# Optimization experiments

Measured on AMD Instinct MI355X. Metric: run time of the kernel, lower is better.

Reference implementation:

```python
import jax, jax.numpy as jnp
import numpy as np

NUM_HEADS = 16
HIDDEN = 64  # per-head dim


def setup_inputs() -> dict:
    key = jax.random.key(0)
    ks = jax.random.split(key, 7)
    B, Nq, S, D = 2, 2048, 2048, 1024
    return {
        "queries": jax.random.normal(ks[0], (B, Nq, D), jnp.float32),
        "keys": jax.random.normal(ks[1], (B, S, D), jnp.float32),
        "values": jax.random.normal(ks[2], (B, S, D), jnp.float32),
        "Wq": jax.random.normal(ks[3], (D, NUM_HEADS * HIDDEN), jnp.float32) * 0.02,
        "Wk": jax.random.normal(ks[4], (D, NUM_HEADS * HIDDEN), jnp.float32) * 0.02,
        "Wv": jax.random.normal(ks[5], (D, NUM_HEADS * HIDDEN), jnp.float32) * 0.02,
        "Wo": jax.random.normal(ks[6], (NUM_HEADS * HIDDEN, 1024), jnp.float32) * 0.02,
    }


def reference(queries, keys, values, Wq, Wk, Wv, Wo):
    B, Nq, _ = queries.shape
    S = keys.shape[1]
    H, dh = NUM_HEADS, HIDDEN
    # projections, split heads: [B, len, H, dh] -> [B, H, len, dh]
    Q = (queries @ Wq).reshape(B, Nq, H, dh).transpose(0, 2, 1, 3)
    K = (keys @ Wk).reshape(B, S, H, dh).transpose(0, 2, 1, 3)
    V = (values @ Wv).reshape(B, S, H, dh).transpose(0, 2, 1, 3)
    scores = jnp.einsum("bhqd,bhkd->bhqk", Q, K) / jnp.sqrt(jnp.float32(dh))
    # NOTE: faithful to original -- softmax over ALL keys, THEN multiply by
    # strictly-lower-triangular mask (triangular * (1 - diagonal)); no renorm.
    P = jax.nn.softmax(scores, axis=-1)
    mask = jnp.tril(jnp.ones((Nq, S), jnp.float32), -1)  # strict lower triangle
    Sout = jnp.einsum("bhqk,bhkd->bhqd", P * mask, V)
    merged = Sout.transpose(0, 2, 1, 3).reshape(B, Nq, H * dh)
    return merged @ Wo
```

## Files before the change

### kernel.cpp

```cpp
#include <hip/hip_runtime.h>
#include <hip/hip_bf16.h>
#include <stdint.h>


typedef __bf16 bf16x8 __attribute__((ext_vector_type(8)));
typedef float f32x4 __attribute__((ext_vector_type(4)));

typedef const __attribute__((address_space(1))) void* gas_t;
typedef __attribute__((address_space(3))) void* las_t;

__device__ __forceinline__ unsigned short f2bf(float f) {
    unsigned int u = __float_as_uint(f);
    return (unsigned short)((u + 0x7FFFu + ((u >> 16) & 1u)) >> 16);
}

__global__ __launch_bounds__(256) void cast_qkv(
    const float* __restrict__ q, const float* __restrict__ k, const float* __restrict__ v,
    unsigned short* __restrict__ oq, unsigned short* __restrict__ ok, unsigned short* __restrict__ ov)
{
    const float* src = (blockIdx.z == 0) ? q : (blockIdx.z == 1) ? k : v;
    unsigned short* dst = (blockIdx.z == 0) ? oq : (blockIdx.z == 1) ? ok : ov;
    unsigned int i = blockIdx.x * 256u + threadIdx.x;
    float4 f = reinterpret_cast<const float4*>(src)[i];
    ushort4 o;
    o.x = f2bf(f.x); o.y = f2bf(f.y); o.z = f2bf(f.z); o.w = f2bf(f.w);
    reinterpret_cast<ushort4*>(dst)[i] = o;
}

__global__ __launch_bounds__(256) void transpose_w(
    const float* __restrict__ w0, const float* __restrict__ w1,
    const float* __restrict__ w2, const float* __restrict__ w3,
    unsigned short* __restrict__ t0, unsigned short* __restrict__ t1,
    unsigned short* __restrict__ t2, unsigned short* __restrict__ t3)
{
    const float* W = (blockIdx.z == 0) ? w0 : (blockIdx.z == 1) ? w1 : (blockIdx.z == 2) ? w2 : w3;
    unsigned short* T = (blockIdx.z == 0) ? t0 : (blockIdx.z == 1) ? t1 : (blockIdx.z == 2) ? t2 : t3;
    __shared__ float s[32][33];
    const int tx = threadIdx.x, ty = threadIdx.y;
    const int x = blockIdx.x * 32 + tx;
#pragma unroll
    for (int j = 0; j < 4; ++j)
        s[ty + 8 * j][tx] = W[(size_t)(blockIdx.y * 32 + ty + 8 * j) * 1024 + x];
    __syncthreads();
    const int xo = blockIdx.y * 32 + tx;
#pragma unroll
    for (int j = 0; j < 4; ++j)
        T[(size_t)(blockIdx.x * 32 + ty + 8 * j) * 1024 + xo] = f2bf(s[tx][ty + 8 * j]);
}

template <int BM, int BN, int MODE>
__global__ __launch_bounds__(256) void gemm_bt(
    const unsigned short* __restrict__ A0, const unsigned short* __restrict__ A1,
    const unsigned short* __restrict__ A2,
    const unsigned short* __restrict__ B0, const unsigned short* __restrict__ B1,
    const unsigned short* __restrict__ B2,
    unsigned short* __restrict__ C0, unsigned short* __restrict__ C1,
    unsigned short* __restrict__ C2, float* __restrict__ Cf)
{
    constexpr int K = 1024;
    constexpr int WM = BM / 2, WN = BN / 2, MI = WM / 16, NI = WN / 16;
    __shared__ __align__(16) unsigned char lds[(BM + BN) * 64];
    unsigned char* lA = lds;
    unsigned char* lB = lds + BM * 64;

    const int tid = threadIdx.x;
    const int z = blockIdx.z;
    const unsigned short* A  = (MODE == 1 || z == 0) ? A0 : (z == 1) ? A1 : A2;
    const unsigned short* Bt = (MODE == 1 || z == 0) ? B0 : (z == 1) ? B1 : B2;
    const int m0 = blockIdx.y * BM, n0 = blockIdx.x * BN;
    const int w = tid >> 6, lane = tid & 63, g = lane >> 4, l15 = lane & 15;
    const int wr = w >> 1, wc = w & 1;

    f32x4 acc[MI][NI] = {};

    for (int k0 = 0; k0 < K; k0 += 32) {
#pragma unroll
        for (int r = 0; r < (BM * 64) / 4096; ++r) {
            const int o = (r * 256 + tid) * 16;
            const unsigned char* gp = (const unsigned char*)A
                + ((size_t)(m0 + (o >> 6)) * K + k0) * 2 + (o & 63);
            __builtin_amdgcn_global_load_lds((gas_t)gp,
                (las_t)(lA + (r * 256 + (tid & ~63)) * 16), 16, 0, 0);
        }
#pragma unroll
        for (int r = 0; r < (BN * 64) / 4096; ++r) {
            const int o = (r * 256 + tid) * 16;
            const unsigned char* gp = (const unsigned char*)Bt
                + ((size_t)(n0 + (o >> 6)) * K + k0) * 2 + (o & 63);
            __builtin_amdgcn_global_load_lds((gas_t)gp,
                (las_t)(lB + (r * 256 + (tid & ~63)) * 16), 16, 0, 0);
        }
        __syncthreads();

        bf16x8 a[MI], bfr[NI];
#pragma unroll
        for (int mi = 0; mi < MI; ++mi)
            a[mi] = *(const bf16x8*)(lA + (wr * WM + mi * 16 + l15) * 64 + g * 16);
#pragma unroll
        for (int ni = 0; ni < NI; ++ni)
            bfr[ni] = *(const bf16x8*)(lB + (wc * WN + ni * 16 + l15) * 64 + g * 16);
#pragma unroll
        for (int mi = 0; mi < MI; ++mi)
#pragma unroll
            for (int ni = 0; ni < NI; ++ni)
                acc[mi][ni] = __builtin_amdgcn_mfma_f32_16x16x32_bf16(a[mi], bfr[ni], acc[mi][ni], 0, 0, 0);
        __syncthreads();
    }

    if (MODE == 1) {
#pragma unroll
        for (int mi = 0; mi < MI; ++mi)
#pragma unroll
            for (int ni = 0; ni < NI; ++ni)
#pragma unroll
                for (int i = 0; i < 4; ++i) {
                    const int row = m0 + wr * WM + mi * 16 + 4 * g + i;
                    const int col = n0 + wc * WN + ni * 16 + l15;
                    Cf[(size_t)row * 1024 + col] = acc[mi][ni][i];
                }
    } else if (z < 2) {
        unsigned short* C = (z == 0) ? C0 : C1;
#pragma unroll
        for (int mi = 0; mi < MI; ++mi)
#pragma unroll
            for (int ni = 0; ni < NI; ++ni)
#pragma unroll
                for (int i = 0; i < 4; ++i) {
                    const int row = m0 + wr * WM + mi * 16 + 4 * g + i;
                    const int col = n0 + wc * WN + ni * 16 + l15;
                    C[(size_t)row * 1024 + col] = f2bf(acc[mi][ni][i]);
                }
    } else {
#pragma unroll
        for (int mi = 0; mi < MI; ++mi)
#pragma unroll
            for (int ni = 0; ni < NI; ++ni)
#pragma unroll
                for (int i = 0; i < 4; ++i) {
                    const int row = m0 + wr * WM + mi * 16 + 4 * g + i;
                    const int col = n0 + wc * WN + ni * 16 + l15;
                    const int b = row >> 11, s = row & 2047;
                    const int hh = col >> 6, d = col & 63;
                    C2[(((size_t)b * 16 + hh) * 64 + d) * 2048 + s] = f2bf(acc[mi][ni][i]);
                }
    }
}

__global__ __launch_bounds__(256) void attn_kernel(
    const unsigned short* __restrict__ Qp, const unsigned short* __restrict__ Kp,
    const unsigned short* __restrict__ Vt, unsigned short* __restrict__ mrg)
{
    __shared__ __align__(16) unsigned char lds[24576];
    unsigned char* Ks = lds;
    unsigned char* Vs = lds + 8192;
    unsigned char* Ps = lds + 16384;

    const int tid = threadIdx.x;
    const int w = tid >> 6, lane = tid & 63, g = lane >> 4, l15 = lane & 15;
    const int qt = blockIdx.x, h = blockIdx.y, b = blockIdx.z;
    const int q0 = qt * 64;
    const int bh = b * 16 + h;

    bf16x8 aq[2];
    {
        const unsigned short* qp = Qp + ((size_t)(b * 2048 + q0 + 16 * w + l15) * 1024 + h * 64 + g * 8);
        aq[0] = *(const bf16x8*)qp;
        aq[1] = *(const bf16x8*)(qp + 32);
    }

    f32x4 oacc[4] = {};
    float denom[4] = {0.f, 0.f, 0.f, 0.f};

    for (int k0 = 0; k0 < 2048; k0 += 64) {
        const bool do_pv = (k0 < q0 + 64);
#pragma unroll
        for (int r = 0; r < 2; ++r) {
            const int o = (r * 256 + tid) * 16;
            const int row = o >> 7;
            const uint4 vv = *(const uint4*)((const unsigned char*)Kp
                + ((size_t)(b * 2048 + k0 + row) * 1024 + h * 64) * 2 + (o & 127));
            *(uint4*)(Ks + (o ^ ((row & 7) << 4))) = vv;
        }
        if (do_pv) {
#pragma unroll
            for (int r = 0; r < 2; ++r) {
                const int o = (r * 256 + tid) * 16;
                const int row = o >> 7;
                const uint4 vv = *(const uint4*)((const unsigned char*)Vt
                    + (((size_t)bh * 64 + row) * 2048 + k0) * 2 + (o & 127));
                *(uint4*)(Vs + (o ^ ((row & 7) << 4))) = vv;
            }
        }
        __syncthreads();

        f32x4 pe[4];
#pragma unroll
        for (int ni = 0; ni < 4; ++ni) {
            const int row = ni * 16 + l15;
            const int sw = (row & 7) << 4;
            const bf16x8 bk0 = *(const bf16x8*)(Ks + ((row * 128 + g * 16) ^ sw));
            const bf16x8 bk1 = *(const bf16x8*)(Ks + ((row * 128 + 64 + g * 16) ^ sw));
            f32x4 t = {};
            t = __builtin_amdgcn_mfma_f32_16x16x32_bf16(aq[0], bk0, t, 0, 0, 0);
            t = __builtin_amdgcn_mfma_f32_16x16x32_bf16(aq[1], bk1, t, 0, 0, 0);
#pragma unroll
            for (int i = 0; i < 4; ++i)
                pe[ni][i] = __expf(t[i] * 0.125f);
        }
#pragma unroll
        for (int i = 0; i < 4; ++i) {
            float rs = pe[0][i] + pe[1][i] + pe[2][i] + pe[3][i];
            rs += __shfl_xor(rs, 1, 64);
            rs += __shfl_xor(rs, 2, 64);
            rs += __shfl_xor(rs, 4, 64);
            rs += __shfl_xor(rs, 8, 64);
            denom[i] += rs;
        }
        if (do_pv) {
#pragma unroll
            for (int ni = 0; ni < 4; ++ni)
#pragma unroll
                for (int i = 0; i < 4; ++i) {
                    const int row = 16 * w + 4 * g + i;
                    const int colg = k0 + ni * 16 + l15;
                    const unsigned short pv =
                        (colg < q0 + row) ? f2bf(pe[ni][i]) : (unsigned short)0;
                    *(unsigned short*)(Ps + ((row * 128 + (ni * 16 + l15) * 2) ^ ((row & 7) << 4))) = pv;
                }
            __syncthreads();
#pragma unroll
            for (int kk = 0; kk < 2; ++kk) {
                const int rowp = 16 * w + l15;
                const bf16x8 pa = *(const bf16x8*)(Ps + ((rowp * 128 + kk * 64 + g * 16) ^ ((rowp & 7) << 4)));
#pragma unroll
                for (int ni = 0; ni < 4; ++ni) {
                    const int rv = ni * 16 + l15;
                    const bf16x8 bv = *(const bf16x8*)(Vs + ((rv * 128 + kk * 64 + g * 16) ^ ((rv & 7) << 4)));
                    oacc[ni] = __builtin_amdgcn_mfma_f32_16x16x32_bf16(pa, bv, oacc[ni], 0, 0, 0);
                }
            }
        }
        __syncthreads();
    }

#pragma unroll
    for (int ni = 0; ni < 4; ++ni)
#pragma unroll
        for (int i = 0; i < 4; ++i) {
            const int row = q0 + 16 * w + 4 * g + i;
            mrg[((size_t)b * 2048 + row) * 1024 + h * 64 + ni * 16 + l15] =
                f2bf(oacc[ni][i] / denom[i]);
        }
}

extern "C" void kernel_launch(void* const* d_in, const int* in_sizes, int n_in,
                              void* d_out, int out_size, void* d_ws, size_t ws_size,
                              hipStream_t stream)
{
    const float* q  = (const float*)d_in[0];
    const float* k  = (const float*)d_in[1];
    const float* v  = (const float*)d_in[2];
    const float* Wq = (const float*)d_in[3];
    const float* Wk = (const float*)d_in[4];
    const float* Wv = (const float*)d_in[5];
    const float* Wo = (const float*)d_in[6];
    float* out = (float*)d_out;

    unsigned short* ws = (unsigned short*)d_ws;
    const size_t TEN = (size_t)2 * 2048 * 1024;
    unsigned short* qbf = ws;
    unsigned short* kbf = ws + TEN;
    unsigned short* vbf = ws + 2 * TEN;
    unsigned short* Wqt = ws + 3 * TEN;
    unsigned short* Wkt = Wqt + 1024 * 1024;
    unsigned short* Wvt = Wkt + 1024 * 1024;
    unsigned short* Wot = Wvt + 1024 * 1024;
    unsigned short* Qp  = ws + 4 * TEN;
    unsigned short* Kp  = ws + 5 * TEN;
    unsigned short* Vtp = ws + 6 * TEN;
    unsigned short* mrg = ws + 7 * TEN;

    cast_qkv<<<dim3(4096, 1, 3), 256, 0, stream>>>(q, k, v, qbf, kbf, vbf);
    transpose_w<<<dim3(32, 32, 4), dim3(32, 8), 0, stream>>>(Wq, Wk, Wv, Wo, Wqt, Wkt, Wvt, Wot);
    gemm_bt<128, 128, 0><<<dim3(8, 32, 3), 256, 0, stream>>>(
        qbf, kbf, vbf, Wqt, Wkt, Wvt, Qp, Kp, Vtp, nullptr);
    attn_kernel<<<dim3(32, 16, 2), 256, 0, stream>>>(Qp, Kp, Vtp, mrg);
    gemm_bt<64, 128, 1><<<dim3(8, 64, 1), 256, 0, stream>>>(
        mrg, nullptr, nullptr, Wot, nullptr, nullptr, nullptr, nullptr, nullptr, out);
}
```

Measured before the change: 273.8 us.

## Split attention into masked PV loop and denominator-only loop, add V transpose kernel

The attention kernel now runs two loops. The first covers the causal key tiles and computes both QK and PV. The second covers the remaining tiles and only computes QK plus exp for the softmax denominator, loading just K with 128-row tiles. Blocks are remapped so the heaviest query tiles launch first, the per-tile warp shuffle reduction is deferred to the end, and the redundant extra barrier is removed. The strided V-transposed store in the projection GEMM is replaced with a coalesced store followed by a separate LDS-based transpose kernel, which adds one launch and extra traffic.

```diff
diff --git a/kernel.cpp b/kernel.cpp
--- a/kernel.cpp
+++ b/kernel.cpp
@@ -46,6 +46,34 @@
 #pragma unroll
     for (int j = 0; j < 4; ++j)
         T[(size_t)(blockIdx.x * 32 + ty + 8 * j) * 1024 + xo] = f2bf(s[tx][ty + 8 * j]);
+}
+
+__global__ __launch_bounds__(256) void transpose_v(
+    const unsigned short* __restrict__ Vp, unsigned short* __restrict__ Vt)
+{
+    __shared__ unsigned short s[64][68];
+    const int tid = threadIdx.x;
+    const int s0 = blockIdx.x * 64, h = blockIdx.y, b = blockIdx.z;
+    const size_t inbase = ((size_t)(b * 2048 + s0)) * 1024 + h * 64;
+#pragma unroll
+    for (int r = 0; r < 4; ++r) {
+        int idx = r * 256 + tid;
+        int row = idx >> 4;
+        int c4 = (idx & 15) * 4;
+        ushort4 v = *(const ushort4*)(Vp + inbase + (size_t)row * 1024 + c4);
+        *(ushort4*)&s[row][c4] = v;
+    }
+    __syncthreads();
+    const size_t outbase = ((size_t)((b * 16 + h) * 64)) * 2048 + s0;
+#pragma unroll
+    for (int r = 0; r < 4; ++r) {
+        int idx = r * 256 + tid;
+        int drow = idx >> 4;
+        int sc = (idx & 15) * 4;
+        ushort4 v;
+        v.x = s[sc][drow]; v.y = s[sc + 1][drow]; v.z = s[sc + 2][drow]; v.w = s[sc + 3][drow];
+        *(ushort4*)(Vt + outbase + (size_t)drow * 2048 + sc) = v;
+    }
 }
 
 template <int BM, int BN, int MODE>
@@ -118,8 +146,8 @@
                     const int col = n0 + wc * WN + ni * 16 + l15;
                     Cf[(size_t)row * 1024 + col] = acc[mi][ni][i];
                 }
-    } else if (z < 2) {
-        unsigned short* C = (z == 0) ? C0 : C1;
+    } else {
+        unsigned short* C = (z == 0) ? C0 : (z == 1) ? C1 : C2;
 #pragma unroll
         for (int mi = 0; mi < MI; ++mi)
 #pragma unroll
@@ -130,20 +158,24 @@
                     const int col = n0 + wc * WN + ni * 16 + l15;
                     C[(size_t)row * 1024 + col] = f2bf(acc[mi][ni][i]);
                 }
-    } else {
-#pragma unroll
-        for (int mi = 0; mi < MI; ++mi)
-#pragma unroll
-            for (int ni = 0; ni < NI; ++ni)
-#pragma unroll
-                for (int i = 0; i < 4; ++i) {
-                    const int row = m0 + wr * WM + mi * 16 + 4 * g + i;
-                    const int col = n0 + wc * WN + ni * 16 + l15;
-                    const int b = row >> 11, s = row & 2047;
-                    const int hh = col >> 6, d = col & 63;
-                    C2[(((size_t)b * 16 + hh) * 64 + d) * 2048 + s] = f2bf(acc[mi][ni][i]);
-                }
-    }
+    }
+}
+
+__device__ __forceinline__ f32x4 qk_exp(const unsigned char* ldsbase, int rowoff,
+                                        int ni, int g, int l15,
+                                        bf16x8 aq0, bf16x8 aq1)
+{
+    const int row = rowoff + ni * 16 + l15;
+    const int sw = (row & 7) << 4;
+    const bf16x8 bk0 = *(const bf16x8*)(ldsbase + ((row * 128 + g * 16) ^ sw));
+    const bf16x8 bk1 = *(const bf16x8*)(ldsbase + ((row * 128 + 64 + g * 16) ^ sw));
+    f32x4 t = {};
+    t = __builtin_amdgcn_mfma_f32_16x16x32_bf16(aq0, bk0, t, 0, 0, 0);
+    t = __builtin_amdgcn_mfma_f32_16x16x32_bf16(aq1, bk1, t, 0, 0, 0);
+    f32x4 r;
+#pragma unroll
+    for (int i = 0; i < 4; ++i) r[i] = __expf(t[i] * 0.125f);
+    return r;
 }
 
 __global__ __launch_bounds__(256) void attn_kernel(
@@ -157,9 +189,11 @@
 
     const int tid = threadIdx.x;
     const int w = tid >> 6, lane = tid & 63, g = lane >> 4, l15 = lane & 15;
-    const int qt = blockIdx.x, h = blockIdx.y, b = blockIdx.z;
+    const int bid = blockIdx.x;
+    const int bh = (bid & 7) * 4 + ((bid >> 3) & 3);
+    const int qt = 31 - (bid >> 5);
+    const int b = bh >> 4, h = bh & 15;
     const int q0 = qt * 64;
-    const int bh = b * 16 + h;
 
     bf16x8 aq[2];
     {
@@ -168,88 +202,102 @@
         aq[1] = *(const bf16x8*)(qp + 32);
     }
 
+    const unsigned char* Kbase = (const unsigned char*)Kp + ((size_t)(b * 2048) * 1024 + h * 64) * 2;
+    const unsigned char* Vbase = (const unsigned char*)Vt + ((size_t)bh * 64) * 2048 * 2;
+
     f32x4 oacc[4] = {};
-    float denom[4] = {0.f, 0.f, 0.f, 0.f};
-
-    for (int k0 = 0; k0 < 2048; k0 += 64) {
-        const bool do_pv = (k0 < q0 + 64);
+    f32x4 dsum = {0.f, 0.f, 0.f, 0.f};
+
+    for (int t = 0; t <= qt; ++t) {
+        const int k0 = t * 64;
 #pragma unroll
         for (int r = 0; r < 2; ++r) {
             const int o = (r * 256 + tid) * 16;
             const int row = o >> 7;
-            const uint4 vv = *(const uint4*)((const unsigned char*)Kp
-                + ((size_t)(b * 2048 + k0 + row) * 1024 + h * 64) * 2 + (o & 127));
-            *(uint4*)(Ks + (o ^ ((row & 7) << 4))) = vv;
-        }
-        if (do_pv) {
-#pragma unroll
-            for (int r = 0; r < 2; ++r) {
-                const int o = (r * 256 + tid) * 16;
-                const int row = o >> 7;
-                const uint4 vv = *(const uint4*)((const unsigned char*)Vt
-                    + (((size_t)bh * 64 + row) * 2048 + k0) * 2 + (o & 127));
-                *(uint4*)(Vs + (o ^ ((row & 7) << 4))) = vv;
+            const uint4 kv = *(const uint4*)(Kbase + (size_t)(k0 + row) * 2048 + (o & 127));
+            *(uint4*)(Ks + (o ^ ((row & 7) << 4))) = kv;
+            const uint4 vv = *(const uint4*)(Vbase + (size_t)row * 4096 + (size_t)k0 * 2 + (o & 127));
+            *(uint4*)(Vs + (o ^ ((row & 7) << 4))) = vv;
+        }
+        __syncthreads();
+
+        f32x4 pe[4];
+#pragma unroll
+        for (int ni = 0; ni < 4; ++ni)
+            pe[ni] = qk_exp(Ks, 0, ni, g, l15, aq[0], aq[1]);
+        dsum += pe[0] + pe[1] + pe[2] + pe[3];
+
+        if (t == qt) {
+#pragma unroll
+            for (int ni = 0; ni < 4; ++ni)
+#pragma unroll
+                for (int i = 0; i < 4; ++i) {
+                    const int rloc = 16 * w + 4 * g + i;
+                    const int kloc = ni * 16 + l15;
+                    const unsigned short pv = (kloc < rloc) ? f2bf(pe[ni][i]) : (unsigned short)0;
+                    *(unsigned short*)(Ps + ((rloc * 128 + kloc * 2) ^ ((rloc & 7) << 4))) = pv;
+                }
+        } else {
+#pragma unroll
+            for (int ni = 0; ni < 4; ++ni)
+#pragma unroll
+                for (int i = 0; i < 4; ++i) {
+                    const int rloc = 16 * w + 4 * g + i;
+                    const int kloc = ni * 16 + l15;
+                    *(unsigned short*)(Ps + ((rloc * 128 + kloc * 2) ^ ((rloc & 7) << 4))) = f2bf(pe[ni][i]);
+                }
+        }
+
+#pragma unroll
+        for (int kk = 0; kk < 2; ++kk) {
+            const int rowp = 16 * w + l15;
+            const bf16x8 pa = *(const bf16x8*)(Ps + ((rowp * 128 + kk * 64 + g * 16) ^ ((rowp & 7) << 4)));
+#pragma unroll
+            for (int ni = 0; ni < 4; ++ni) {
+                const int rv = ni * 16 + l15;
+                const bf16x8 bv = *(const bf16x8*)(Vs + ((rv * 128 + kk * 64 + g * 16) ^ ((rv & 7) << 4)));
+                oacc[ni] = __builtin_amdgcn_mfma_f32_16x16x32_bf16(pa, bv, oacc[ni], 0, 0, 0);
             }
         }
         __syncthreads();
-
-        f32x4 pe[4];
-#pragma unroll
-        for (int ni = 0; ni < 4; ++ni) {
-            const int row = ni * 16 + l15;
-            const int sw = (row & 7) << 4;
-            const bf16x8 bk0 = *(const bf16x8*)(Ks + ((row * 128 + g * 16) ^ sw));
-            const bf16x8 bk1 = *(const bf16x8*)(Ks + ((row * 128 + 64 + g * 16) ^ sw));
-            f32x4 t = {};
-            t = __builtin_amdgcn_mfma_f32_16x16x32_bf16(aq[0], bk0, t, 0, 0, 0);
-            t = __builtin_amdgcn_mfma_f32_16x16x32_bf16(aq[1], bk1, t, 0, 0, 0);
-#pragma unroll
-            for (int i = 0; i < 4; ++i)
-                pe[ni][i] = __expf(t[i] * 0.125f);
-        }
-#pragma unroll
-        for (int i = 0; i < 4; ++i) {
-            float rs = pe[0][i] + pe[1][i] + pe[2][i] + pe[3][i];
-            rs += __shfl_xor(rs, 1, 64);
-            rs += __shfl_xor(rs, 2, 64);
-            rs += __shfl_xor(rs, 4, 64);
-            rs += __shfl_xor(rs, 8, 64);
-            denom[i] += rs;
-        }
-        if (do_pv) {
-#pragma unroll
-            for (int ni = 0; ni < 4; ++ni)
-#pragma unroll
-                for (int i = 0; i < 4; ++i) {
-                    const int row = 16 * w + 4 * g + i;
-                    const int colg = k0 + ni * 16 + l15;
-                    const unsigned short pv =
-                        (colg < q0 + row) ? f2bf(pe[ni][i]) : (unsigned short)0;
-                    *(unsigned short*)(Ps + ((row * 128 + (ni * 16 + l15) * 2) ^ ((row & 7) << 4))) = pv;
-                }
-            __syncthreads();
-#pragma unroll
-            for (int kk = 0; kk < 2; ++kk) {
-                const int rowp = 16 * w + l15;
-                const bf16x8 pa = *(const bf16x8*)(Ps + ((rowp * 128 + kk * 64 + g * 16) ^ ((rowp & 7) << 4)));
-#pragma unroll
-                for (int ni = 0; ni < 4; ++ni) {
-                    const int rv = ni * 16 + l15;
-                    const bf16x8 bv = *(const bf16x8*)(Vs + ((rv * 128 + kk * 64 + g * 16) ^ ((rv & 7) << 4)));
-                    oacc[ni] = __builtin_amdgcn_mfma_f32_16x16x32_bf16(pa, bv, oacc[ni], 0, 0, 0);
-                }
+    }
+
+    for (int k0 = (qt + 1) * 64; k0 < 2048; k0 += 128) {
+        const int nk = min(128, 2048 - k0);
+        for (int r = 0; r < (nk >> 5); ++r) {
+            const int o = (r * 256 + tid) * 16;
+            const int row = o >> 7;
+            *(uint4*)(lds + (o ^ ((row & 7) << 4))) =
+                *(const uint4*)(Kbase + (size_t)(k0 + row) * 2048 + (o & 127));
+        }
+        __syncthreads();
+        for (int koff = 0; koff < nk; koff += 64) {
+#pragma unroll
+            for (int ni = 0; ni < 4; ++ni) {
+                f32x4 pe = qk_exp(lds, koff, ni, g, l15, aq[0], aq[1]);
+                dsum += pe;
             }
         }
         __syncthreads();
     }
 
+    float den[4];
+#pragma unroll
+    for (int i = 0; i < 4; ++i) {
+        float rs = dsum[i];
+        rs += __shfl_xor(rs, 1, 64);
+        rs += __shfl_xor(rs, 2, 64);
+        rs += __shfl_xor(rs, 4, 64);
+        rs += __shfl_xor(rs, 8, 64);
+        den[i] = rs;
+    }
 #pragma unroll
     for (int ni = 0; ni < 4; ++ni)
 #pragma unroll
         for (int i = 0; i < 4; ++i) {
             const int row = q0 + 16 * w + 4 * g + i;
             mrg[((size_t)b * 2048 + row) * 1024 + h * 64 + ni * 16 + l15] =
-                f2bf(oacc[ni][i] / denom[i]);
+                f2bf(oacc[ni][i] / den[i]);
         }
 }
 
@@ -277,14 +325,16 @@
     unsigned short* Wot = Wvt + 1024 * 1024;
     unsigned short* Qp  = ws + 4 * TEN;
     unsigned short* Kp  = ws + 5 * TEN;
-    unsigned short* Vtp = ws + 6 * TEN;
-    unsigned short* mrg = ws + 7 * TEN;
+    unsigned short* Vp  = ws + 6 * TEN;
+    unsigned short* Vt  = qbf;
+    unsigned short* mrg = kbf;
 
     cast_qkv<<<dim3(4096, 1, 3), 256, 0, stream>>>(q, k, v, qbf, kbf, vbf);
     transpose_w<<<dim3(32, 32, 4), dim3(32, 8), 0, stream>>>(Wq, Wk, Wv, Wo, Wqt, Wkt, Wvt, Wot);
     gemm_bt<128, 128, 0><<<dim3(8, 32, 3), 256, 0, stream>>>(
-        qbf, kbf, vbf, Wqt, Wkt, Wvt, Qp, Kp, Vtp, nullptr);
-    attn_kernel<<<dim3(32, 16, 2), 256, 0, stream>>>(Qp, Kp, Vtp, mrg);
+        qbf, kbf, vbf, Wqt, Wkt, Wvt, Qp, Kp, Vp, nullptr);
+    transpose_v<<<dim3(32, 16, 2), 256, 0, stream>>>(Vp, Vt);
+    attn_kernel<<<dim3(1024, 1, 1), 256, 0, stream>>>(Qp, Kp, Vt, mrg);
     gemm_bt<64, 128, 1><<<dim3(8, 64, 1), 256, 0, stream>>>(
         mrg, nullptr, nullptr, Wot, nullptr, nullptr, nullptr, nullptr, nullptr, out);
 }
```

New measurement: 232.9 us. -15.0%, faster.
